# Optimization experiments

Hardware: AMD Instinct MI355X
Metric: run time of the kernel (lower is better)

The kernel has to match this reference:

```python
import jax, jax.numpy as jnp
import numpy as np

W_FLOAT = 13.7
W_CEIL = 14                      # int(ceil(w))
RGB_IDX = (3, 7, 10)             # round(w/4), round(w/2), round(3w/4)


def setup_inputs() -> dict:
    key = jax.random.key(0)
    B, H, W = 1, 2048, 3072
    x = jax.random.uniform(key, (B, 1, H, W), jnp.float32)
    # lenticule-start mask: one start every w_ceil columns (periodic), so every
    # spreader window of width w_ceil contains exactly one start (z_norm >= 1)
    z = (jnp.arange(W) % W_CEIL == 0).astype(jnp.float32)
    z = jnp.broadcast_to(z[None, None, None, :], (B, 1, H, W)).copy()
    return {"x": x, "z": z}


def _moving_sum(a, win):
    cs = jnp.cumsum(a, axis=-1)
    shifted = jnp.concatenate([jnp.zeros_like(cs[..., :win]), cs[..., :-win]], axis=-1)
    return cs - shifted


def _forward(x, z):
    B, _, H, W = x.shape
    # --- Space2Features: the eye/delay one-hot convs are a pure shift-gather:
    # x_exp[b,i,h,p] = x[b,0,h,p+i] * z[b,0,h,p]
    xp = jnp.pad(x, ((0, 0), (0, 0), (0, 0), (0, W_CEIL - 1)))
    idx = jnp.arange(W)[None, :] + jnp.arange(W_CEIL)[:, None]        # [w_ceil, W]
    x_shift = jnp.moveaxis(jnp.take(xp, idx, axis=3)[:, 0], 2, 1)     # [B, w_ceil, H, W]
    x_exp = x_shift * z                                               # gate by mask
    # --- RGBExtractor_fixed (autotune off): RGB is one-hot over the channel
    # dim, so the 1x1 conv is channel selection at the fixed R/G/B offsets
    x_rgb = x_exp[:, jnp.array(RGB_IDX)]                              # [B, 3, H, W]
    # rgb_filter_image[b,c,h,p] = z[b,0,h,p - idx_c]  (right-shift of mask)
    zp = jnp.pad(z, ((0, 0), (0, 0), (0, 0), (W_CEIL - 1, 0)))
    ridx = jnp.arange(W)[None, :] - jnp.array(RGB_IDX)[:, None] + (W_CEIL - 1)  # [3, W]
    rgb_filter_image = jnp.moveaxis(jnp.take(zp, ridx, axis=3)[:, 0], 2, 1)     # [B,3,H,W]
    # --- LenticuleSpreader: per-channel backward moving sum of width w_ceil,
    # then normalize by the spread mask
    y = _moving_sum(x_rgb, W_CEIL) / _moving_sum(z, W_CEIL)
    return y, rgb_filter_image


def reference(x, z):
    return _forward(x, z)
```

## Files before the change

kernel.cpp:

```cpp
#include <hip/hip_runtime.h>

constexpr int Wd  = 3072;
constexpr int WC  = 14;
constexpr int XL  = 12;
constexpr int XR  = 16;
constexpr int ZL  = 16;

__global__ __launch_bounds__(256)
void color_restore_kernel(const float* __restrict__ xg,
                          const float* __restrict__ zg,
                          float* __restrict__ out, int Hn)
{
    __shared__ __align__(16) float xs[XL + Wd + XR];
    __shared__ __align__(16) float zs[ZL + Wd];

    const int h = blockIdx.x;
    const int t = threadIdx.x;

    const float4* xrow = (const float4*)(xg + (size_t)h * Wd);
    const float4* zrow = (const float4*)(zg + (size_t)h * Wd);
    float4* xs4 = (float4*)(xs + XL);
    float4* zs4 = (float4*)(zs + ZL);
#pragma unroll
    for (int i = 0; i < 3; ++i) {
        const int idx = t + i * 256;
        xs4[idx] = xrow[idx];
        zs4[idx] = zrow[idx];
    }
    if (t < XL) xs[t] = 0.f;
    if (t < XR) xs[XL + Wd + t] = 0.f;
    if (t < ZL) zs[t] = 0.f;
    __syncthreads();

    const int plane = Hn * Wd;
    float* yout = out;
    float* rout = out + 3 * (size_t)plane;

#pragma unroll
    for (int p = 0; p < 3; ++p) {
        const int w0 = p * 1024 + 4 * t;

        float zbuf[20];
        {
            float4* zb = (float4*)zbuf;
            const int zblk = (ZL + w0 - 13) >> 2;
#pragma unroll
            for (int i = 0; i < 5; ++i) zb[i] = ((const float4*)zs)[zblk + i];
        }
        float xbuf[28];
        {
            float4* xb = (float4*)xbuf;
            const int xblk = (XL + w0 - 10) >> 2;
#pragma unroll
            for (int i = 0; i < 7; ++i) xb[i] = ((const float4*)xs)[xblk + i];
        }

        float den = 0.f, n0 = 0.f, n1 = 0.f, n2 = 0.f;
#pragma unroll
        for (int s = 0; s < WC; ++s) {
            const float zj = zbuf[3 + s];
            den += zj;
            n0 = fmaf(xbuf[s + 2], zj, n0);
            n1 = fmaf(xbuf[s + 6], zj, n1);
            n2 = fmaf(xbuf[s + 9], zj, n2);
        }

        float y0[4], y1[4], y2[4], r0[4], r1[4], r2[4];
#pragma unroll
        for (int q = 0; q < 4; ++q) {
            if (q > 0) {
                const float zin  = zbuf[16 + q];
                const float zot  = zbuf[2 + q];
                den += zin - zot;
                n0 += xbuf[15 + q] * zin - xbuf[1 + q] * zot;
                n1 += xbuf[19 + q] * zin - xbuf[5 + q] * zot;
                n2 += xbuf[22 + q] * zin - xbuf[8 + q] * zot;
            }
            const float rinv = __builtin_amdgcn_rcpf(den);
            y0[q] = n0 * rinv;
            y1[q] = n1 * rinv;
            y2[q] = n2 * rinv;
            r0[q] = zbuf[13 + q];
            r1[q] = zbuf[9 + q];
            r2[q] = zbuf[6 + q];
        }

        const int off = h * Wd + w0;
        *(float4*)(yout + off)             = make_float4(y0[0], y0[1], y0[2], y0[3]);
        *(float4*)(yout + plane + off)     = make_float4(y1[0], y1[1], y1[2], y1[3]);
        *(float4*)(yout + 2 * plane + off) = make_float4(y2[0], y2[1], y2[2], y2[3]);
        *(float4*)(rout + off)             = make_float4(r0[0], r0[1], r0[2], r0[3]);
        *(float4*)(rout + plane + off)     = make_float4(r1[0], r1[1], r1[2], r1[3]);
        *(float4*)(rout + 2 * plane + off) = make_float4(r2[0], r2[1], r2[2], r2[3]);
    }
}

extern "C" void kernel_launch(void* const* d_in, const int* in_sizes, int n_in,
                              void* d_out, int out_size, void* d_ws, size_t ws_size,
                              hipStream_t stream)
{
    const float* x = (const float*)d_in[0];
    const float* z = (const float*)d_in[1];
    float* out = (float*)d_out;
    const int Hn = in_sizes[0] / Wd;
    color_restore_kernel<<<dim3(Hn), dim3(256), 0, stream>>>(x, z, out, Hn);
}
```

Before: 189.0 us.

## Split each row into three segment blocks with halo loads

Each block now handles one 1024-column segment of a row instead of a whole row, tripling the grid to 3×H blocks. Each block loads its segment plus small left and right halos of x and z into smaller shared buffers. The aim is more blocks in flight, better occupancy and latency hiding, and less shared memory per block. The cost is some redundant halo loads and more block launches.

```diff
diff --git a/kernel.cpp b/kernel.cpp
--- a/kernel.cpp
+++ b/kernel.cpp
@@ -1,98 +1,96 @@
 #include <hip/hip_runtime.h>
 
 constexpr int Wd  = 3072;
+constexpr int SEG = 1024;
 constexpr int WC  = 14;
-constexpr int XL  = 12;
-constexpr int XR  = 16;
-constexpr int ZL  = 16;
 
 __global__ __launch_bounds__(256)
 void color_restore_kernel(const float* __restrict__ xg,
                           const float* __restrict__ zg,
                           float* __restrict__ out, int Hn)
 {
-    __shared__ __align__(16) float xs[XL + Wd + XR];
-    __shared__ __align__(16) float zs[ZL + Wd];
+    __shared__ __align__(16) float xs[SEG + 32];
+    __shared__ __align__(16) float zs[SEG + 16];
 
-    const int h = blockIdx.x;
-    const int t = threadIdx.x;
+    const int p  = blockIdx.x;
+    const int h  = blockIdx.y;
+    const int t  = threadIdx.x;
+    const int c0 = p * SEG;
 
     const float4* xrow = (const float4*)(xg + (size_t)h * Wd);
     const float4* zrow = (const float4*)(zg + (size_t)h * Wd);
-    float4* xs4 = (float4*)(xs + XL);
-    float4* zs4 = (float4*)(zs + ZL);
+    float4* xs4 = (float4*)xs;
+    float4* zs4 = (float4*)zs;
+    const int b0 = c0 >> 2;
+
+    xs4[4 + t] = xrow[b0 + t];
+    zs4[4 + t] = zrow[b0 + t];
+    const float4 zero4 = make_float4(0.f, 0.f, 0.f, 0.f);
+    if (t < 4) {
+        const int c4 = b0 - 4 + t;
+        xs4[t] = (c4 >= 0) ? xrow[c4] : zero4;
+    } else if (t < 8) {
+        const int i = t - 4, c4 = b0 + (SEG >> 2) + i;
+        xs4[4 + (SEG >> 2) + i] = (c4 < (Wd >> 2)) ? xrow[c4] : zero4;
+    } else if (t < 12) {
+        const int i = t - 8, c4 = b0 - 4 + i;
+        zs4[i] = (c4 >= 0) ? zrow[c4] : zero4;
+    }
+    __syncthreads();
+
+    float zbuf[20];
+    {
+        float4* zb = (float4*)zbuf;
 #pragma unroll
-    for (int i = 0; i < 3; ++i) {
-        const int idx = t + i * 256;
-        xs4[idx] = xrow[idx];
-        zs4[idx] = zrow[idx];
+        for (int i = 0; i < 5; ++i) zb[i] = zs4[t + i];
     }
-    if (t < XL) xs[t] = 0.f;
-    if (t < XR) xs[XL + Wd + t] = 0.f;
-    if (t < ZL) zs[t] = 0.f;
-    __syncthreads();
+    float xbuf[28];
+    {
+        float4* xb = (float4*)xbuf;
+#pragma unroll
+        for (int i = 0; i < 7; ++i) xb[i] = xs4[t + 1 + i];
+    }
+
+    float den = 0.f, n0 = 0.f, n1 = 0.f, n2 = 0.f;
+#pragma unroll
+    for (int s = 0; s < WC; ++s) {
+        const float zj = zbuf[3 + s];
+        den += zj;
+        n0 = fmaf(xbuf[s + 2], zj, n0);
+        n1 = fmaf(xbuf[s + 6], zj, n1);
+        n2 = fmaf(xbuf[s + 9], zj, n2);
+    }
+
+    float y0[4], y1[4], y2[4], r0[4], r1[4], r2[4];
+#pragma unroll
+    for (int q = 0; q < 4; ++q) {
+        if (q > 0) {
+            const float zin = zbuf[16 + q];
+            const float zot = zbuf[2 + q];
+            den += zin - zot;
+            n0 += xbuf[15 + q] * zin - xbuf[1 + q] * zot;
+            n1 += xbuf[19 + q] * zin - xbuf[5 + q] * zot;
+            n2 += xbuf[22 + q] * zin - xbuf[8 + q] * zot;
+        }
+        const float rinv = __builtin_amdgcn_rcpf(den);
+        y0[q] = n0 * rinv;
+        y1[q] = n1 * rinv;
+        y2[q] = n2 * rinv;
+        r0[q] = zbuf[13 + q];
+        r1[q] = zbuf[9 + q];
+        r2[q] = zbuf[6 + q];
+    }
 
     const int plane = Hn * Wd;
     float* yout = out;
     float* rout = out + 3 * (size_t)plane;
-
-#pragma unroll
-    for (int p = 0; p < 3; ++p) {
-        const int w0 = p * 1024 + 4 * t;
-
-        float zbuf[20];
-        {
-            float4* zb = (float4*)zbuf;
-            const int zblk = (ZL + w0 - 13) >> 2;
-#pragma unroll
-            for (int i = 0; i < 5; ++i) zb[i] = ((const float4*)zs)[zblk + i];
-        }
-        float xbuf[28];
-        {
-            float4* xb = (float4*)xbuf;
-            const int xblk = (XL + w0 - 10) >> 2;
-#pragma unroll
-            for (int i = 0; i < 7; ++i) xb[i] = ((const float4*)xs)[xblk + i];
-        }
-
-        float den = 0.f, n0 = 0.f, n1 = 0.f, n2 = 0.f;
-#pragma unroll
-        for (int s = 0; s < WC; ++s) {
-            const float zj = zbuf[3 + s];
-            den += zj;
-            n0 = fmaf(xbuf[s + 2], zj, n0);
-            n1 = fmaf(xbuf[s + 6], zj, n1);
-            n2 = fmaf(xbuf[s + 9], zj, n2);
-        }
-
-        float y0[4], y1[4], y2[4], r0[4], r1[4], r2[4];
-#pragma unroll
-        for (int q = 0; q < 4; ++q) {
-            if (q > 0) {
-                const float zin  = zbuf[16 + q];
-                const float zot  = zbuf[2 + q];
-                den += zin - zot;
-                n0 += xbuf[15 + q] * zin - xbuf[1 + q] * zot;
-                n1 += xbuf[19 + q] * zin - xbuf[5 + q] * zot;
-                n2 += xbuf[22 + q] * zin - xbuf[8 + q] * zot;
-            }
-            const float rinv = __builtin_amdgcn_rcpf(den);
-            y0[q] = n0 * rinv;
-            y1[q] = n1 * rinv;
-            y2[q] = n2 * rinv;
-            r0[q] = zbuf[13 + q];
-            r1[q] = zbuf[9 + q];
-            r2[q] = zbuf[6 + q];
-        }
-
-        const int off = h * Wd + w0;
-        *(float4*)(yout + off)             = make_float4(y0[0], y0[1], y0[2], y0[3]);
-        *(float4*)(yout + plane + off)     = make_float4(y1[0], y1[1], y1[2], y1[3]);
-        *(float4*)(yout + 2 * plane + off) = make_float4(y2[0], y2[1], y2[2], y2[3]);
-        *(float4*)(rout + off)             = make_float4(r0[0], r0[1], r0[2], r0[3]);
-        *(float4*)(rout + plane + off)     = make_float4(r1[0], r1[1], r1[2], r1[3]);
-        *(float4*)(rout + 2 * plane + off) = make_float4(r2[0], r2[1], r2[2], r2[3]);
-    }
+    const int off = h * Wd + c0 + 4 * t;
+    *(float4*)(yout + off)             = make_float4(y0[0], y0[1], y0[2], y0[3]);
+    *(float4*)(yout + plane + off)     = make_float4(y1[0], y1[1], y1[2], y1[3]);
+    *(float4*)(yout + 2 * plane + off) = make_float4(y2[0], y2[1], y2[2], y2[3]);
+    *(float4*)(rout + off)             = make_float4(r0[0], r0[1], r0[2], r0[3]);
+    *(float4*)(rout + plane + off)     = make_float4(r1[0], r1[1], r1[2], r1[3]);
+    *(float4*)(rout + 2 * plane + off) = make_float4(r2[0], r2[1], r2[2], r2[3]);
 }
 
 extern "C" void kernel_launch(void* const* d_in, const int* in_sizes, int n_in,
@@ -103,5 +101,5 @@
     const float* z = (const float*)d_in[1];
     float* out = (float*)d_out;
     const int Hn = in_sizes[0] / Wd;
-    color_restore_kernel<<<dim3(Hn), dim3(256), 0, stream>>>(x, z, out, Hn);
+    color_restore_kernel<<<dim3(3, Hn), dim3(256), 0, stream>>>(x, z, out, Hn);
 }
```

Result: no change. 190.8 us (+1.0%).
